# Kernel tuning notes

Hardware: AMD Instinct MI355X
Metric: run time of the kernel (lower is better)

The kernel has to match this reference:

```python
import jax, jax.numpy as jnp
import numpy as np

B, T, C = 8, 2048, 768
H = 1  # n_heads
EPS = 1e-5


def layer_norm(x, g, b):
    mu = jnp.mean(x, axis=-1, keepdims=True)
    var = jnp.mean(jnp.square(x - mu), axis=-1, keepdims=True)
    return (x - mu) * jax.lax.rsqrt(var + EPS) * g + b


def setup_inputs() -> dict:
    key = jax.random.key(0)
    ks = jax.random.split(key, 12)
    s = 1.0 / np.sqrt(C)
    return {
        "x": jax.random.normal(ks[0], (B, T, C), jnp.float32),
        "Wq": jax.random.normal(ks[1], (C, C), jnp.float32) * s,
        "Wk": jax.random.normal(ks[2], (C, C), jnp.float32) * s,
        "Wv": jax.random.normal(ks[3], (C, C), jnp.float32) * s,
        "Wp": jax.random.normal(ks[4], (C, C), jnp.float32) * s,
        "bp": jnp.zeros((C,), jnp.float32),
        "g1": jnp.ones((C,), jnp.float32),
        "b1": jnp.zeros((C,), jnp.float32),
        "g2": jnp.ones((C,), jnp.float32),
        "b2": jnp.zeros((C,), jnp.float32),
        "W1": jax.random.normal(ks[5], (C, 4 * C), jnp.float32) * s,
        "bm1": jnp.zeros((4 * C,), jnp.float32),
        "W2": jax.random.normal(ks[6], (4 * C, C), jnp.float32) * (1.0 / np.sqrt(4 * C)),
        "bm2": jnp.zeros((C,), jnp.float32),
    }


def attention(xn, Wq, Wk, Wv, Wp, bp):
    # single head (H=1): q,k,v are [B, T, C]
    q = xn @ Wq
    k = xn @ Wk
    v = xn @ Wv
    scale = 1.0 / np.sqrt(C // H)
    scores = jnp.einsum("btc,bsc->bts", q, k) * scale  # [B,T,T]
    causal = jnp.tril(jnp.ones((T, T), dtype=bool))
    scores = jnp.where(causal, scores, -jnp.inf)
    attn = jax.nn.softmax(scores, axis=-1)
    y = jnp.einsum("bts,bsc->btc", attn, v)
    return y @ Wp + bp


def reference(x, Wq, Wk, Wv, Wp, bp, g1, b1, g2, b2, W1, bm1, W2, bm2):
    # pre-LN transformer block; dropout is identity at eval
    x = x + attention(layer_norm(x, g1, b1), Wq, Wk, Wv, Wp, bp)
    h = layer_norm(x, g2, b2)
    h = jax.nn.gelu(h @ W1 + bm1, approximate=False) @ W2 + bm2
    return x + h
```

## Files before the change

### kernel.cpp

```cpp
#include <hip/hip_runtime.h>
#include <hip/hip_bf16.h>


typedef unsigned short u16;
typedef __bf16 bf16x8 __attribute__((ext_vector_type(8)));
typedef float  f32x4  __attribute__((ext_vector_type(4)));
typedef float  f32x16 __attribute__((ext_vector_type(16)));
typedef int    i32x4  __attribute__((ext_vector_type(4)));
typedef u16    u16x4  __attribute__((ext_vector_type(4)));
typedef u16    u16x8  __attribute__((ext_vector_type(8)));

__device__ __forceinline__ u16 f2b(float f) {
    __hip_bfloat16 h = __float2bfloat16(f);
    return *reinterpret_cast<u16*>(&h);
}
__device__ __forceinline__ float b2f(u16 u) {
    unsigned int x = ((unsigned int)u) << 16;
    return __uint_as_float(x);
}

__device__ __forceinline__ float fast_gelu(float v) {
    float t = v * v;
    float z = v * fmaf(0.10294294f, t, 2.30211842f);
    float e = exp2f(-z);
    return v * __builtin_amdgcn_rcpf(1.0f + e);
}

__device__ __forceinline__ void stage16(u16* lds_base_uniform, const u16* g, int lane) {
#if __has_builtin(__builtin_amdgcn_global_load_lds)
    __builtin_amdgcn_global_load_lds(
        (const __attribute__((address_space(1))) void*)g,
        (__attribute__((address_space(3))) void*)lds_base_uniform,
        16, 0, 0);
#else
    *(i32x4*)(lds_base_uniform + lane * 8) = *(const i32x4*)g;
#endif
}

__global__ __launch_bounds__(256) void transpose_cast(const float* __restrict__ in,
                                                      u16* __restrict__ out,
                                                      int R, int Cc) {
    __shared__ float tile[32][33];
    int c0 = blockIdx.x * 32, r0 = blockIdx.y * 32;
    int tx = threadIdx.x, ty = threadIdx.y;
    for (int i = ty; i < 32; i += 8)
        tile[i][tx] = in[(long)(r0 + i) * Cc + c0 + tx];
    __syncthreads();
    for (int i = ty; i < 32; i += 8)
        out[(long)(c0 + i) * R + r0 + tx] = f2b(tile[tx][i]);
}

__global__ __launch_bounds__(192) void ln_kernel(const float* __restrict__ x,
                                                 const float* __restrict__ g,
                                                 const float* __restrict__ b,
                                                 u16* __restrict__ out) {
    const int C = 768;
    long row = blockIdx.x;
    const float* xr = x + row * C;
    int t = threadIdx.x;
    f32x4 v = *(const f32x4*)(xr + t * 4);
    float s = v[0] + v[1] + v[2] + v[3];
    float sq = v[0] * v[0] + v[1] * v[1] + v[2] * v[2] + v[3] * v[3];
#pragma unroll
    for (int o = 32; o; o >>= 1) {
        s += __shfl_xor(s, o);
        sq += __shfl_xor(sq, o);
    }
    __shared__ float ss[3], sq2[3];
    int wv = t >> 6;
    if ((t & 63) == 0) { ss[wv] = s; sq2[wv] = sq; }
    __syncthreads();
    s = ss[0] + ss[1] + ss[2];
    sq = sq2[0] + sq2[1] + sq2[2];
    float mu = s * (1.0f / 768.0f);
    float var = sq * (1.0f / 768.0f) - mu * mu;
    float rs = rsqrtf(var + 1e-5f);
    f32x4 gv = *(const f32x4*)(g + t * 4);
    f32x4 bv = *(const f32x4*)(b + t * 4);
    u16x4 pk;
#pragma unroll
    for (int j = 0; j < 4; j++) pk[j] = f2b((v[j] - mu) * rs * gv[j] + bv[j]);
    *(u16x4*)(out + row * C + t * 4) = pk;
}

__global__ __launch_bounds__(256) void softmax_causal(u16* __restrict__ S) {
    const int T = 2048;
    long row = blockIdx.x;
    int t = (int)(row & (T - 1));
    int ncols = ((t >> 7) + 1) << 7;
    u16* p = S + row * T;
    int tid = threadIdx.x;
    int base = tid * 8;
    bool act = base < ncols;
    float v[8];
    float mx = -3.0e38f;
    if (act) {
        u16x8 raw = *(const u16x8*)(p + base);
#pragma unroll
        for (int j = 0; j < 8; j++) {
            int col = base + j;
            v[j] = (col <= t) ? b2f(raw[j]) : -3.0e38f;
            mx = fmaxf(mx, v[j]);
        }
    }
#pragma unroll
    for (int o = 32; o; o >>= 1) mx = fmaxf(mx, __shfl_xor(mx, o));
    __shared__ float sm[4], ssum[4];
    int wv = tid >> 6;
    if ((tid & 63) == 0) sm[wv] = mx;
    __syncthreads();
    mx = fmaxf(fmaxf(sm[0], sm[1]), fmaxf(sm[2], sm[3]));
    float s = 0.0f;
    if (act) {
#pragma unroll
        for (int j = 0; j < 8; j++) {
            int col = base + j;
            float e = (col <= t) ? __expf(v[j] - mx) : 0.0f;
            v[j] = e;
            s += e;
        }
    }
#pragma unroll
    for (int o = 32; o; o >>= 1) s += __shfl_xor(s, o);
    if ((tid & 63) == 0) ssum[wv] = s;
    __syncthreads();
    s = ssum[0] + ssum[1] + ssum[2] + ssum[3];
    float inv = 1.0f / s;
    if (act) {
        u16x8 pk;
#pragma unroll
        for (int j = 0; j < 8; j++) pk[j] = f2b(v[j] * inv);
        *(u16x8*)(p + base) = pk;
    }
}

#define BM 128
#define BN 128
#define BKT 64

template <int EPI, int CAUSAL>
__global__ __launch_bounds__(256, 4) void gemm_bt(const u16* __restrict__ A,
                                                  const u16* __restrict__ Bt,
                                                  void* __restrict__ Out,
                                                  void* __restrict__ Out2,
                                                  const float* __restrict__ bias,
                                                  const float* __restrict__ resid,
                                                  int M, int N, int K,
                                                  int lda, int ldb, int ldo,
                                                  long long sA, long long sB, long long sO,
                                                  float scale) {
    int bz = blockIdx.z;
    A += (long)bz * sA;
    Bt += (long)bz * sB;
    long obase = (long)bz * sO;

    int gx = gridDim.x;
    int nblk = gx * gridDim.y;
    int lin = blockIdx.y * gx + blockIdx.x;
    int chunk = nblk >> 3;
    int tile = (lin & 7) * chunk + (lin >> 3);
    int m0 = (tile / gx) * BM;
    int n0 = (tile % gx) * BN;

    if (CAUSAL == 1 && n0 >= m0 + BM) return;
    int kend = (CAUSAL == 2) ? ((K < m0 + BM) ? K : (m0 + BM)) : K;

    __shared__ __align__(16) u16 As[128 * 64];
    __shared__ __align__(16) u16 Bs[128 * 64];

    int tid = threadIdx.x;
    int lane = tid & 63;
    int l32 = lane & 31, kg = lane >> 5;
    int w = tid >> 6;
    int wm = (w >> 1) * 64, wn = (w & 1) * 64;

    f32x16 acc[2][2] = {};

    for (int k0 = 0; k0 < kend; k0 += BKT) {
#pragma unroll
        for (int i = 0; i < 4; i++) {
            int ebase = i * 256 + w * 64;
            int e = ebase + lane;
            int row = e >> 3;
            int gc = (e & 7) ^ (row & 7);
            stage16(As + ebase * 8, A + (long)(m0 + row) * lda + k0 + gc * 8, lane);
            stage16(Bs + ebase * 8, Bt + (long)(n0 + row) * ldb + k0 + gc * 8, lane);
        }
        __syncthreads();
#pragma unroll
        for (int kk = 0; kk < 4; kk++) {
            int c = (kk << 1) + kg;
            bf16x8 af[2], bf[2];
#pragma unroll
            for (int mt = 0; mt < 2; mt++) {
                int r = wm + mt * 32 + l32;
                af[mt] = *(const bf16x8*)(As + r * 64 + ((c ^ (r & 7)) << 3));
            }
#pragma unroll
            for (int nt = 0; nt < 2; nt++) {
                int r = wn + nt * 32 + l32;
                bf[nt] = *(const bf16x8*)(Bs + r * 64 + ((c ^ (r & 7)) << 3));
            }
#pragma unroll
            for (int mt = 0; mt < 2; mt++)
#pragma unroll
                for (int nt = 0; nt < 2; nt++)
                    acc[mt][nt] = __builtin_amdgcn_mfma_f32_32x32x16_bf16(af[mt], bf[nt], acc[mt][nt], 0, 0, 0);
        }
        __syncthreads();
    }

#pragma unroll
    for (int mt = 0; mt < 2; ++mt)
#pragma unroll
        for (int nt = 0; nt < 2; ++nt) {
            int col = n0 + wn + nt * 32 + l32;
            int rb = m0 + wm + mt * 32 + 4 * kg;
            f32x16 a = acc[mt][nt];
            if (EPI == 0) {
                u16* o = (u16*)Out + obase;
#pragma unroll
                for (int r = 0; r < 16; r++)
                    o[(long)(rb + (r & 3) + 8 * (r >> 2)) * ldo + col] = f2b(a[r] * scale);
            } else if (EPI == 2) {
                u16* o = (u16*)Out + obase;
                float bv = bias[col];
#pragma unroll
                for (int r = 0; r < 16; r++)
                    o[(long)(rb + (r & 3) + 8 * (r >> 2)) * ldo + col] = f2b(fast_gelu(a[r] + bv));
            } else if (EPI == 3) {
                float* o = (float*)Out + obase;
                float bv = bias[col];
#pragma unroll
                for (int r = 0; r < 16; r++) {
                    long idx = (long)(rb + (r & 3) + 8 * (r >> 2)) * ldo + col;
                    o[idx] = resid[idx] + a[r] + bv;
                }
            } else {
                if (col < 1536) {
                    u16* o = (u16*)Out;
#pragma unroll
                    for (int r = 0; r < 16; r++)
                        o[(long)(rb + (r & 3) + 8 * (r >> 2)) * 1536 + col] = f2b(a[r]);
                } else {
                    u16* o = (u16*)Out2;
                    int c = col - 1536;
#pragma unroll
                    for (int gi = 0; gi < 4; gi++) {
                        int row = rb + 8 * gi;
                        int b = row >> 11, t = row & 2047;
                        u16x4 pk;
#pragma unroll
                        for (int j = 0; j < 4; j++) pk[j] = f2b(a[gi * 4 + j]);
                        *(u16x4*)(o + ((long)b * 768 + c) * 2048 + t) = pk;
                    }
                }
            }
        }
}

extern "C" void kernel_launch(void* const* d_in, const int* in_sizes, int n_in,
                              void* d_out, int out_size, void* d_ws, size_t ws_size,
                              hipStream_t stream) {
    (void)in_sizes; (void)n_in; (void)out_size; (void)ws_size;
    const float* x   = (const float*)d_in[0];
    const float* Wq  = (const float*)d_in[1];
    const float* Wk  = (const float*)d_in[2];
    const float* Wv  = (const float*)d_in[3];
    const float* Wp  = (const float*)d_in[4];
    const float* bp  = (const float*)d_in[5];
    const float* g1  = (const float*)d_in[6];
    const float* b1  = (const float*)d_in[7];
    const float* g2  = (const float*)d_in[8];
    const float* b2  = (const float*)d_in[9];
    const float* W1  = (const float*)d_in[10];
    const float* bm1 = (const float*)d_in[11];
    const float* W2  = (const float*)d_in[12];
    const float* bm2 = (const float*)d_in[13];
    float* out = (float*)d_out;

    const int Bn = 8, T = 2048, C = 768, F = 3072;
    const int M = Bn * T;

    char* ws = (char*)d_ws;
    u16* xn = (u16*)(ws);
    u16* QK = (u16*)(ws + 25165824);
    u16* vT = (u16*)(ws + 75497472);
    u16* S  = (u16*)(ws + 100663296);
    u16* y  = (u16*)(ws + 167772160);
    u16* h1 = (u16*)(ws + 25165824);
    u16* wgt = (u16*)(ws + 192937984);
    u16* Wqt = wgt;
    u16* Wkt = Wqt + 589824;
    u16* Wvt = Wkt + 589824;
    u16* Wpt = Wvt + 589824;
    u16* W1t = Wpt + 589824;
    u16* W2t = W1t + (long)C * F;

    dim3 tb(32, 8);
    hipLaunchKernelGGL(transpose_cast, dim3(C / 32, C / 32), tb, 0, stream, Wq, Wqt, C, C);
    hipLaunchKernelGGL(transpose_cast, dim3(C / 32, C / 32), tb, 0, stream, Wk, Wkt, C, C);
    hipLaunchKernelGGL(transpose_cast, dim3(C / 32, C / 32), tb, 0, stream, Wv, Wvt, C, C);
    hipLaunchKernelGGL(transpose_cast, dim3(C / 32, C / 32), tb, 0, stream, Wp, Wpt, C, C);
    hipLaunchKernelGGL(transpose_cast, dim3(F / 32, C / 32), tb, 0, stream, W1, W1t, C, F);
    hipLaunchKernelGGL(transpose_cast, dim3(C / 32, F / 32), tb, 0, stream, W2, W2t, F, C);

    hipLaunchKernelGGL(ln_kernel, dim3(M), dim3(192), 0, stream, x, g1, b1, xn);

    hipLaunchKernelGGL((gemm_bt<4, 0>), dim3((3 * C) / BN, M / BM, 1), dim3(256), 0, stream,
                       xn, Wqt, (void*)QK, (void*)vT, nullptr, nullptr,
                       M, 3 * C, C, C, C, 0, 0LL, 0LL, 0LL, 1.0f);

    float scl = 1.0f / sqrtf((float)C);
    hipLaunchKernelGGL((gemm_bt<0, 1>), dim3(T / BN, T / BM, Bn), dim3(256), 0, stream,
                       QK, QK + 768, (void*)S, nullptr, nullptr, nullptr,
                       T, T, C, 1536, 1536, T,
                       (long long)T * 1536, (long long)T * 1536, (long long)T * T, scl);

    hipLaunchKernelGGL(softmax_causal, dim3(M), dim3(256), 0, stream, S);

    hipLaunchKernelGGL((gemm_bt<0, 2>), dim3(C / BN, T / BM, Bn), dim3(256), 0, stream,
                       S, vT, (void*)y, nullptr, nullptr, nullptr,
                       T, C, T, T, T, C,
                       (long long)T * T, (long long)C * T, (long long)T * C, 1.0f);

    hipLaunchKernelGGL((gemm_bt<3, 0>), dim3(C / BN, M / BM, 1), dim3(256), 0, stream,
                       y, Wpt, (void*)out, nullptr, bp, x,
                       M, C, C, C, C, C, 0LL, 0LL, 0LL, 1.0f);

    hipLaunchKernelGGL(ln_kernel, dim3(M), dim3(192), 0, stream, out, g2, b2, xn);

    hipLaunchKernelGGL((gemm_bt<2, 0>), dim3(F / BN, M / BM, 1), dim3(256), 0, stream,
                       xn, W1t, (void*)h1, nullptr, bm1, nullptr,
                       M, F, C, C, C, F, 0LL, 0LL, 0LL, 1.0f);

    hipLaunchKernelGGL((gemm_bt<3, 0>), dim3(C / BN, M / BM, 1), dim3(256), 0, stream,
                       h1, W2t, (void*)out, nullptr, bm2, out,
                       M, C, F, F, F, C, 0LL, 0LL, 0LL, 1.0f);
}
```

Before: 608.1 us.

## Fuse prep kernels, add bf16 residual copy for LN2, and refine LDS swizzle

```diff
diff --git a/kernel.cpp b/kernel.cpp
--- a/kernel.cpp
+++ b/kernel.cpp
@@ -37,12 +37,16 @@
 #endif
 }
 
-__global__ __launch_bounds__(256) void transpose_cast(const float* __restrict__ in,
-                                                      u16* __restrict__ out,
-                                                      int R, int Cc) {
+struct PrepArgs {
+    const float *x, *g1, *b1, *Wq, *Wk, *Wv, *Wp, *W1, *W2;
+    u16 *xn, *Wqt, *Wkt, *Wvt, *Wpt, *W1t, *W2t;
+};
+
+__device__ __forceinline__ void do_transpose(const float* in, u16* out, int R, int Cc,
+                                             int bx, int by, int tid) {
     __shared__ float tile[32][33];
-    int c0 = blockIdx.x * 32, r0 = blockIdx.y * 32;
-    int tx = threadIdx.x, ty = threadIdx.y;
+    int c0 = bx * 32, r0 = by * 32;
+    int tx = tid & 31, ty = tid >> 5;
     for (int i = ty; i < 32; i += 8)
         tile[i][tx] = in[(long)(r0 + i) * Cc + c0 + tx];
     __syncthreads();
@@ -50,22 +54,62 @@
         out[(long)(c0 + i) * R + r0 + tx] = f2b(tile[tx][i]);
 }
 
-__global__ __launch_bounds__(192) void ln_kernel(const float* __restrict__ x,
-                                                 const float* __restrict__ g,
-                                                 const float* __restrict__ b,
-                                                 u16* __restrict__ out) {
+__global__ __launch_bounds__(256) void prep_kernel(PrepArgs a) {
+    int z = blockIdx.x;
+    int tid = threadIdx.x;
+    if (z < 16384) {
+        const int C = 768;
+        const float* xr = a.x + (long)z * C;
+        float v0 = xr[tid], v1 = xr[tid + 256], v2 = xr[tid + 512];
+        float s = v0 + v1 + v2;
+        float sq = v0 * v0 + v1 * v1 + v2 * v2;
+#pragma unroll
+        for (int o = 32; o; o >>= 1) { s += __shfl_xor(s, o); sq += __shfl_xor(sq, o); }
+        __shared__ float ss[4], sq2[4];
+        int wv = tid >> 6;
+        if ((tid & 63) == 0) { ss[wv] = s; sq2[wv] = sq; }
+        __syncthreads();
+        s = ss[0] + ss[1] + ss[2] + ss[3];
+        sq = sq2[0] + sq2[1] + sq2[2] + sq2[3];
+        float mu = s * (1.0f / 768.0f);
+        float var = sq * (1.0f / 768.0f) - mu * mu;
+        float rs = rsqrtf(var + 1e-5f);
+        u16* orow = a.xn + (long)z * C;
+        orow[tid]       = f2b((v0 - mu) * rs * a.g1[tid]       + a.b1[tid]);
+        orow[tid + 256] = f2b((v1 - mu) * rs * a.g1[tid + 256] + a.b1[tid + 256]);
+        orow[tid + 512] = f2b((v2 - mu) * rs * a.g1[tid + 512] + a.b1[tid + 512]);
+    } else {
+        int t = z - 16384;
+        if (t < 2304) {
+            int m = t / 576, tt = t % 576;
+            const float* in = (m == 0) ? a.Wq : (m == 1) ? a.Wk : (m == 2) ? a.Wv : a.Wp;
+            u16* out = (m == 0) ? a.Wqt : (m == 1) ? a.Wkt : (m == 2) ? a.Wvt : a.Wpt;
+            do_transpose(in, out, 768, 768, tt % 24, tt / 24, tid);
+        } else if (t < 4608) {
+            int tt = t - 2304;
+            do_transpose(a.W1, a.W1t, 768, 3072, tt % 96, tt / 96, tid);
+        } else {
+            int tt = t - 4608;
+            do_transpose(a.W2, a.W2t, 3072, 768, tt % 24, tt / 24, tid);
+        }
+    }
+}
+
+__global__ __launch_bounds__(192) void ln2_kernel(const u16* __restrict__ xb,
+                                                  const float* __restrict__ g,
+                                                  const float* __restrict__ b,
+                                                  u16* __restrict__ out) {
     const int C = 768;
     long row = blockIdx.x;
-    const float* xr = x + row * C;
     int t = threadIdx.x;
-    f32x4 v = *(const f32x4*)(xr + t * 4);
+    u16x4 raw = *(const u16x4*)(xb + row * C + t * 4);
+    f32x4 v;
+#pragma unroll
+    for (int j = 0; j < 4; j++) v[j] = b2f(raw[j]);
     float s = v[0] + v[1] + v[2] + v[3];
     float sq = v[0] * v[0] + v[1] * v[1] + v[2] * v[2] + v[3] * v[3];
 #pragma unroll
-    for (int o = 32; o; o >>= 1) {
-        s += __shfl_xor(s, o);
-        sq += __shfl_xor(sq, o);
-    }
+    for (int o = 32; o; o >>= 1) { s += __shfl_xor(s, o); sq += __shfl_xor(sq, o); }
     __shared__ float ss[3], sq2[3];
     int wv = t >> 6;
     if ((t & 63) == 0) { ss[wv] = s; sq2[wv] = sq; }
@@ -174,6 +218,11 @@
     int w = tid >> 6;
     int wm = (w >> 1) * 64, wn = (w & 1) * 64;
 
+    int rA0 = wm + l32, rA1 = wm + 32 + l32;
+    int rB0 = wn + l32, rB1 = wn + 32 + l32;
+    int swA0 = (rA0 & 7) ^ ((rA0 >> 3) & 3), swA1 = (rA1 & 7) ^ ((rA1 >> 3) & 3);
+    int swB0 = (rB0 & 7) ^ ((rB0 >> 3) & 3), swB1 = (rB1 & 7) ^ ((rB1 >> 3) & 3);
+
     f32x16 acc[2][2] = {};
 
     for (int k0 = 0; k0 < kend; k0 += BKT) {
@@ -182,7 +231,7 @@
             int ebase = i * 256 + w * 64;
             int e = ebase + lane;
             int row = e >> 3;
-            int gc = (e & 7) ^ (row & 7);
+            int gc = (e & 7) ^ (row & 7) ^ ((row >> 3) & 3);
             stage16(As + ebase * 8, A + (long)(m0 + row) * lda + k0 + gc * 8, lane);
             stage16(Bs + ebase * 8, Bt + (long)(n0 + row) * ldb + k0 + gc * 8, lane);
         }
@@ -191,16 +240,10 @@
         for (int kk = 0; kk < 4; kk++) {
             int c = (kk << 1) + kg;
             bf16x8 af[2], bf[2];
-#pragma unroll
-            for (int mt = 0; mt < 2; mt++) {
-                int r = wm + mt * 32 + l32;
-                af[mt] = *(const bf16x8*)(As + r * 64 + ((c ^ (r & 7)) << 3));
-            }
-#pragma unroll
-            for (int nt = 0; nt < 2; nt++) {
-                int r = wn + nt * 32 + l32;
-                bf[nt] = *(const bf16x8*)(Bs + r * 64 + ((c ^ (r & 7)) << 3));
-            }
+            af[0] = *(const bf16x8*)(As + rA0 * 64 + ((c ^ swA0) << 3));
+            af[1] = *(const bf16x8*)(As + rA1 * 64 + ((c ^ swA1) << 3));
+            bf[0] = *(const bf16x8*)(Bs + rB0 * 64 + ((c ^ swB0) << 3));
+            bf[1] = *(const bf16x8*)(Bs + rB1 * 64 + ((c ^ swB1) << 3));
 #pragma unroll
             for (int mt = 0; mt < 2; mt++)
 #pragma unroll
@@ -228,13 +271,16 @@
 #pragma unroll
                 for (int r = 0; r < 16; r++)
                     o[(long)(rb + (r & 3) + 8 * (r >> 2)) * ldo + col] = f2b(fast_gelu(a[r] + bv));
-            } else if (EPI == 3) {
+            } else if (EPI == 3 || EPI == 5) {
                 float* o = (float*)Out + obase;
+                u16* o2 = (u16*)Out2;
                 float bv = bias[col];
 #pragma unroll
                 for (int r = 0; r < 16; r++) {
                     long idx = (long)(rb + (r & 3) + 8 * (r >> 2)) * ldo + col;
-                    o[idx] = resid[idx] + a[r] + bv;
+                    float val = resid[idx] + a[r] + bv;
+                    o[idx] = val;
+                    if (EPI == 5) o2[idx] = f2b(val);
                 }
             } else {
                 if (col < 1536) {
@@ -287,6 +333,7 @@
     u16* QK = (u16*)(ws + 25165824);
     u16* vT = (u16*)(ws + 75497472);
     u16* S  = (u16*)(ws + 100663296);
+    u16* xb = (u16*)(ws + 100663296);
     u16* y  = (u16*)(ws + 167772160);
     u16* h1 = (u16*)(ws + 25165824);
     u16* wgt = (u16*)(ws + 192937984);
@@ -297,15 +344,8 @@
     u16* W1t = Wpt + 589824;
     u16* W2t = W1t + (long)C * F;
 
-    dim3 tb(32, 8);
-    hipLaunchKernelGGL(transpose_cast, dim3(C / 32, C / 32), tb, 0, stream, Wq, Wqt, C, C);
-    hipLaunchKernelGGL(transpose_cast, dim3(C / 32, C / 32), tb, 0, stream, Wk, Wkt, C, C);
-    hipLaunchKernelGGL(transpose_cast, dim3(C / 32, C / 32), tb, 0, stream, Wv, Wvt, C, C);
-    hipLaunchKernelGGL(transpose_cast, dim3(C / 32, C / 32), tb, 0, stream, Wp, Wpt, C, C);
-    hipLaunchKernelGGL(transpose_cast, dim3(F / 32, C / 32), tb, 0, stream, W1, W1t, C, F);
-    hipLaunchKernelGGL(transpose_cast, dim3(C / 32, F / 32), tb, 0, stream, W2, W2t, F, C);
-
-    hipLaunchKernelGGL(ln_kernel, dim3(M), dim3(192), 0, stream, x, g1, b1, xn);
+    PrepArgs pa{x, g1, b1, Wq, Wk, Wv, Wp, W1, W2, xn, Wqt, Wkt, Wvt, Wpt, W1t, W2t};
+    hipLaunchKernelGGL(prep_kernel, dim3(16384 + 6912), dim3(256), 0, stream, pa);
 
     hipLaunchKernelGGL((gemm_bt<4, 0>), dim3((3 * C) / BN, M / BM, 1), dim3(256), 0, stream,
                        xn, Wqt, (void*)QK, (void*)vT, nullptr, nullptr,
@@ -324,11 +364,11 @@
                        T, C, T, T, T, C,
                        (long long)T * T, (long long)C * T, (long long)T * C, 1.0f);
 
-    hipLaunchKernelGGL((gemm_bt<3, 0>), dim3(C / BN, M / BM, 1), dim3(256), 0, stream,
-                       y, Wpt, (void*)out, nullptr, bp, x,
+    hipLaunchKernelGGL((gemm_bt<5, 0>), dim3(C / BN, M / BM, 1), dim3(256), 0, stream,
+                       y, Wpt, (void*)out, (void*)xb, bp, x,
                        M, C, C, C, C, C, 0LL, 0LL, 0LL, 1.0f);
 
-    hipLaunchKernelGGL(ln_kernel, dim3(M), dim3(192), 0, stream, out, g2, b2, xn);
+    hipLaunchKernelGGL(ln2_kernel, dim3(M), dim3(192), 0, stream, xb, g2, b2, xn);
 
     hipLaunchKernelGGL((gemm_bt<2, 0>), dim3(F / BN, M / BM, 1), dim3(256), 0, stream,
                        xn, W1t, (void*)h1, nullptr, bm1, nullptr,
```

Measured after the change: 649.1 us. +6.7%, slower.
